# Kernel optimization log

Measured on AMD Instinct MI355X. Metric: run time of the kernel, lower is better.

The kernel has to match this reference:

```python
import jax, jax.numpy as jnp
import numpy as np

B = 64      # batch
T = 32      # frames per clip
H = 256     # hidden_dim
NMAX = 64   # max boxes per batch element


def _n_per_frame():
    rng = np.random.default_rng(0)
    return rng.integers(32, NMAX + 1, size=B)  # each n <= NMAX


def setup_inputs() -> dict:
    n = _n_per_frame()
    N = int(n.sum())  # total boxes across batch (~3072)
    key = jax.random.key(0)
    k1, k2, k3 = jax.random.split(key, 3)
    bbox = jax.random.uniform(k1, (N * T, 4), dtype=jnp.float32)
    W1 = jax.random.normal(k2, (4, 128), dtype=jnp.float32) * 0.5
    b1 = jnp.zeros((128,), jnp.float32)
    W2 = jax.random.normal(k3, (128, H), dtype=jnp.float32) * 0.0884  # ~1/sqrt(128)
    b2 = jnp.zeros((H,), jnp.float32)
    return {
        "bbox": bbox,
        "W1": W1, "b1": b1, "W2": W2, "b2": b2,
        "n_per_frame": jnp.asarray(n, jnp.int32),
        "n_max": NMAX,
    }


def reference(bbox, W1, b1, W2, b2, n_per_frame, n_max):
    N = bbox.shape[0] // T  # static total box count
    # tiny MLP: 4 -> 128 -> H
    pos = (jax.nn.relu(bbox @ W1 + b1) @ W2 + b2).reshape(N, T, H)
    # ragged scatter into padded (B*n_max, T, H) tensor
    frame_id = jnp.repeat(jnp.arange(B), n_per_frame, total_repeat_length=N)  # [N]
    starts = jnp.cumsum(n_per_frame) - n_per_frame                            # exclusive cumsum [B]
    local = jnp.arange(N) - starts[frame_id]                                  # slot within frame
    tgt = frame_id * n_max + local                                            # [N] unique targets
    pos_pad = jnp.zeros((B * n_max, T, H), pos.dtype).at[tgt].set(pos)
    # (B, n_max, T, H) -> (B, T, n_max, H) -> (B*T, n_max, H) -> (n_max, B*T, H)
    out = (pos_pad.reshape(B, n_max, T, H)
           .transpose(0, 2, 1, 3)
           .reshape(B * T, n_max, H)
           .transpose(1, 0, 2))
    return out
```

## Files before the change

### kernel.cpp

```cpp
#include <hip/hip_runtime.h>

#define B_ 64
#define T_ 32
#define H_ 256
#define NMAX_ 64
#define GRID 2048
#define BLOCK 256
#define HSROW 136

typedef __attribute__((ext_vector_type(8))) short short8;
typedef __attribute__((ext_vector_type(4))) float f32x4;

__device__ __forceinline__ short f2bf(float f) {
    unsigned u = __builtin_bit_cast(unsigned, f);
    u = (u + 0x7fffu + ((u >> 16) & 1u)) >> 16;
    return (short)u;
}

__device__ __forceinline__ void barrier_nodrain() {
    asm volatile("s_waitcnt lgkmcnt(0)\n\ts_barrier" ::: "memory");
}

__global__ __launch_bounds__(BLOCK, 4)
void pe_fused(const float* __restrict__ bbox,
              const float* __restrict__ W1,
              const float* __restrict__ b1,
              const float* __restrict__ W2,
              const float* __restrict__ b2,
              const int*   __restrict__ npf,
              float* __restrict__ out,
              int NT)
{
    __shared__ float4 W1t[128];
    __shared__ float  b1s[128];
    __shared__ int    s_n[64];
    __shared__ int    s_start[64];
    __shared__ short  Hs[64 * HSROW];

    const int tid  = threadIdx.x;
    const int wave = tid >> 6;
    const int lane = tid & 63;
    const int q    = lane >> 4;
    const int m16  = lane & 15;

    const int ch = blockIdx.x & 1;
    const int p0 = blockIdx.x >> 1;

    if (tid < 128) {
        W1t[tid] = make_float4(W1[tid], W1[128 + tid], W1[256 + tid], W1[384 + tid]);
        b1s[tid] = b1[tid];
    }
    if (wave == 0) {
        int v = npf[lane];
        s_n[lane] = v;
        int s = v;
#pragma unroll
        for (int d = 1; d < 64; d <<= 1) {
            int u = __shfl_up(s, d, 64);
            if (lane >= d) s += u;
        }
        s_start[lane] = s - v;
    }

    const int colw = ch * 128 + wave * 32;
    short8 Wf[2][4];
#pragma unroll
    for (int ct = 0; ct < 2; ++ct)
#pragma unroll
        for (int kc = 0; kc < 4; ++kc) {
            short8 f;
#pragma unroll
            for (int jj = 0; jj < 8; ++jj)
                f[jj] = f2bf(W2[(kc * 32 + q * 8 + jj) * H_ + colw + ct * 16 + m16]);
            Wf[ct][kc] = f;
        }
    float4 b2v[2];
#pragma unroll
    for (int ct = 0; ct < 2; ++ct)
        b2v[ct] = *(const float4*)(b2 + colw + ct * 16 + q * 4);

    barrier_nodrain();

#pragma unroll
    for (int it = 0; it < 2; ++it) {
        const int pair = it ? (p0 + 1024) : p0;
        const int b    = pair >> 5;
        const int l0   = (pair & 31) * 2;
        const int nb   = s_n[b];

        const int ob0 = (l0 * (B_ * T_) + b * T_) * H_;
        const int ob1 = ob0 + (B_ * T_) * H_;

        if (l0 >= nb) {
            const float4 z = make_float4(0.f, 0.f, 0.f, 0.f);
            const int col = ch * 128 + (lane & 31) * 4;
#pragma unroll
            for (int j = 0; j < 8; ++j) {
                const int r = wave * 16 + j * 2 + (lane >> 5);
                float* dst = out + (r < 32 ? ob0 + r * H_ : ob1 + (r - 32) * H_) + col;
                *(float4*)dst = z;
            }
            continue;
        }

        barrier_nodrain();

        {
            const int r4 = tid >> 2;
            const int c4 = tid & 3;
            const int g  = (s_start[b] + l0) * T_ + r4;
            float4 bv = make_float4(0.f, 0.f, 0.f, 0.f);
            if (g < NT) bv = *(const float4*)(bbox + g * 4);
            short* hrow = &Hs[r4 * HSROW + c4 * 32];
#pragma unroll
            for (int w = 0; w < 4; ++w) {
                short8 hv;
#pragma unroll
                for (int jj = 0; jj < 8; ++jj) {
                    const int h = c4 * 32 + w * 8 + jj;
                    const float4 wv = W1t[h];
                    float v = b1s[h];
                    v = fmaf(bv.x, wv.x, v);
                    v = fmaf(bv.y, wv.y, v);
                    v = fmaf(bv.z, wv.z, v);
                    v = fmaf(bv.w, wv.w, v);
                    v = fmaxf(v, 0.f);
                    hv[jj] = f2bf(v);
                }
                *(short8*)(hrow + w * 8) = hv;
            }
        }
        barrier_nodrain();

        f32x4 acc[2][4];
#pragma unroll
        for (int ct = 0; ct < 2; ++ct)
#pragma unroll
            for (int rt = 0; rt < 4; ++rt)
                acc[ct][rt] = (f32x4){b2v[ct].x, b2v[ct].y, b2v[ct].z, b2v[ct].w};

#pragma unroll
        for (int kc = 0; kc < 4; ++kc) {
            short8 hf[4];
#pragma unroll
            for (int rt = 0; rt < 4; ++rt)
                hf[rt] = *(const short8*)&Hs[(rt * 16 + m16) * HSROW + kc * 32 + q * 8];
#pragma unroll
            for (int ct = 0; ct < 2; ++ct)
#pragma unroll
                for (int rt = 0; rt < 4; ++rt)
                    acc[ct][rt] = __builtin_amdgcn_mfma_f32_16x16x32_bf16(
                        Wf[ct][kc], hf[rt], acc[ct][rt], 0, 0, 0);
        }

        const bool v1 = (l0 + 1) < nb;
#pragma unroll
        for (int ct = 0; ct < 2; ++ct) {
            const int cb = colw + ct * 16 + q * 4;
#pragma unroll
            for (int rt = 0; rt < 4; ++rt) {
                const int t = (rt & 1) * 16 + m16;
                float* dst = out + (rt < 2 ? ob0 : ob1) + t * H_ + cb;
                float4 val;
                if (rt >= 2 && !v1) {
                    val = make_float4(0.f, 0.f, 0.f, 0.f);
                } else {
                    const f32x4 a = acc[ct][rt];
                    val = make_float4(a[0], a[1], a[2], a[3]);
                }
                *(float4*)dst = val;
            }
        }
    }
}

extern "C" void kernel_launch(void* const* d_in, const int* in_sizes, int n_in,
                              void* d_out, int out_size, void* d_ws, size_t ws_size,
                              hipStream_t stream)
{
    const float* bbox = (const float*)d_in[0];
    const float* W1   = (const float*)d_in[1];
    const float* b1   = (const float*)d_in[2];
    const float* W2   = (const float*)d_in[3];
    const float* b2   = (const float*)d_in[4];
    const int*   npf  = (const int*)d_in[5];
    const int NT = in_sizes[0] / 4;

    pe_fused<<<GRID, BLOCK, 0, stream>>>(bbox, W1, b1, W2, b2, npf,
                                         (float*)d_out, NT);
}
```

Before: 165.4 us.

## Use 512-thread blocks covering all hidden columns and register-resident W1

Blocks grow from 256 to 512 threads so each block covers all 256 output columns instead of splitting them across two blocks. This halves the grid and removes the duplicated first-layer MLP work per box pair. W1 and b1 now live in registers per lane (two hidden units per lane) instead of in shared memory. The first-layer results are written to shared memory as packed bf16 pairs, and the barrier moves to after the MFMA reads. Occupancy may drop because of the larger block and the extra registers, and the store pattern changes.

```diff
diff --git a/kernel.cpp b/kernel.cpp
--- a/kernel.cpp
+++ b/kernel.cpp
@@ -4,17 +4,16 @@
 #define T_ 32
 #define H_ 256
 #define NMAX_ 64
-#define GRID 2048
-#define BLOCK 256
+#define GRID 1024
+#define BLOCK 512
 #define HSROW 136
 
 typedef __attribute__((ext_vector_type(8))) short short8;
 typedef __attribute__((ext_vector_type(4))) float f32x4;
 
-__device__ __forceinline__ short f2bf(float f) {
+__device__ __forceinline__ unsigned f2bfbits(float f) {
     unsigned u = __builtin_bit_cast(unsigned, f);
-    u = (u + 0x7fffu + ((u >> 16) & 1u)) >> 16;
-    return (short)u;
+    return (u + 0x7fffu + ((u >> 16) & 1u)) >> 16;
 }
 
 __device__ __forceinline__ void barrier_nodrain() {
@@ -31,11 +30,9 @@
               float* __restrict__ out,
               int NT)
 {
-    __shared__ float4 W1t[128];
-    __shared__ float  b1s[128];
-    __shared__ int    s_n[64];
-    __shared__ int    s_start[64];
-    __shared__ short  Hs[64 * HSROW];
+    __shared__ int   s_n[64];
+    __shared__ int   s_start[64];
+    __shared__ short Hs[64 * HSROW];
 
     const int tid  = threadIdx.x;
     const int wave = tid >> 6;
@@ -43,13 +40,6 @@
     const int q    = lane >> 4;
     const int m16  = lane & 15;
 
-    const int ch = blockIdx.x & 1;
-    const int p0 = blockIdx.x >> 1;
-
-    if (tid < 128) {
-        W1t[tid] = make_float4(W1[tid], W1[128 + tid], W1[256 + tid], W1[384 + tid]);
-        b1s[tid] = b1[tid];
-    }
     if (wave == 0) {
         int v = npf[lane];
         s_n[lane] = v;
@@ -62,72 +52,76 @@
         s_start[lane] = s - v;
     }
 
-    const int colw = ch * 128 + wave * 32;
+    const int h0 = lane * 2;
+    float w1a[4], w1b[4];
+#pragma unroll
+    for (int x = 0; x < 4; ++x) {
+        w1a[x] = W1[x * 128 + h0];
+        w1b[x] = W1[x * 128 + h0 + 1];
+    }
+    const float b1a = b1[h0], b1b = b1[h0 + 1];
+
+    const int colw = wave * 32;
     short8 Wf[2][4];
 #pragma unroll
     for (int ct = 0; ct < 2; ++ct)
 #pragma unroll
         for (int kc = 0; kc < 4; ++kc) {
+            const int k0 = kc * 32 + q * 8;
             short8 f;
 #pragma unroll
             for (int jj = 0; jj < 8; ++jj)
-                f[jj] = f2bf(W2[(kc * 32 + q * 8 + jj) * H_ + colw + ct * 16 + m16]);
+                f[jj] = (short)f2bfbits(W2[(k0 + jj) * H_ + colw + ct * 16 + m16]);
             Wf[ct][kc] = f;
         }
-    float4 b2v[2];
+    float4 bq[2];
 #pragma unroll
     for (int ct = 0; ct < 2; ++ct)
-        b2v[ct] = *(const float4*)(b2 + colw + ct * 16 + q * 4);
+        bq[ct] = *(const float4*)(b2 + colw + ct * 16 + q * 4);
 
-    barrier_nodrain();
+    __syncthreads();
 
 #pragma unroll
-    for (int it = 0; it < 2; ++it) {
-        const int pair = it ? (p0 + 1024) : p0;
-        const int b    = pair >> 5;
-        const int l0   = (pair & 31) * 2;
-        const int nb   = s_n[b];
+    for (int i = 0; i < 2; ++i) {
+        const int tt = blockIdx.x + i * GRID;
+        const int b  = tt >> 5;
+        const int l0 = (tt & 31) * 2;
+        const int nb = s_n[b];
 
         const int ob0 = (l0 * (B_ * T_) + b * T_) * H_;
         const int ob1 = ob0 + (B_ * T_) * H_;
 
         if (l0 >= nb) {
             const float4 z = make_float4(0.f, 0.f, 0.f, 0.f);
-            const int col = ch * 128 + (lane & 31) * 4;
 #pragma unroll
-            for (int j = 0; j < 8; ++j) {
-                const int r = wave * 16 + j * 2 + (lane >> 5);
-                float* dst = out + (r < 32 ? ob0 + r * H_ : ob1 + (r - 32) * H_) + col;
-                *(float4*)dst = z;
+            for (int rr = 0; rr < 8; ++rr) {
+                const int r = wave * 8 + rr;
+                float* dst = out + (r < 32 ? ob0 + r * H_ : ob1 + (r - 32) * H_);
+                *(float4*)(dst + lane * 4) = z;
             }
             continue;
         }
 
-        barrier_nodrain();
-
         {
-            const int r4 = tid >> 2;
-            const int c4 = tid & 3;
-            const int g  = (s_start[b] + l0) * T_ + r4;
-            float4 bv = make_float4(0.f, 0.f, 0.f, 0.f);
-            if (g < NT) bv = *(const float4*)(bbox + g * 4);
-            short* hrow = &Hs[r4 * HSROW + c4 * 32];
+            const int gbase = (s_start[b] + l0) * T_ + wave * 8;
+            float4 bx[8];
 #pragma unroll
-            for (int w = 0; w < 4; ++w) {
-                short8 hv;
+            for (int k = 0; k < 8; ++k) {
+                const int g = gbase + k;
+                bx[k] = make_float4(0.f, 0.f, 0.f, 0.f);
+                if (g < NT) bx[k] = *(const float4*)(bbox + g * 4);
+            }
 #pragma unroll
-                for (int jj = 0; jj < 8; ++jj) {
-                    const int h = c4 * 32 + w * 8 + jj;
-                    const float4 wv = W1t[h];
-                    float v = b1s[h];
-                    v = fmaf(bv.x, wv.x, v);
-                    v = fmaf(bv.y, wv.y, v);
-                    v = fmaf(bv.z, wv.z, v);
-                    v = fmaf(bv.w, wv.w, v);
-                    v = fmaxf(v, 0.f);
-                    hv[jj] = f2bf(v);
-                }
-                *(short8*)(hrow + w * 8) = hv;
+            for (int k = 0; k < 8; ++k) {
+                const float4 bv = bx[k];
+                float va = b1a, vb = b1b;
+                va = fmaf(bv.x, w1a[0], va); vb = fmaf(bv.x, w1b[0], vb);
+                va = fmaf(bv.y, w1a[1], va); vb = fmaf(bv.y, w1b[1], vb);
+                va = fmaf(bv.z, w1a[2], va); vb = fmaf(bv.z, w1b[2], vb);
+                va = fmaf(bv.w, w1a[3], va); vb = fmaf(bv.w, w1b[3], vb);
+                va = fmaxf(va, 0.f);         vb = fmaxf(vb, 0.f);
+                const unsigned packed = f2bfbits(va) | (f2bfbits(vb) << 16);
+                *(unsigned*)&Hs[(wave * 8 + k) * HSROW + h0] = packed;
             }
         }
         barrier_nodrain();
@@ -137,7 +131,7 @@
         for (int ct = 0; ct < 2; ++ct)
 #pragma unroll
             for (int rt = 0; rt < 4; ++rt)
-                acc[ct][rt] = (f32x4){b2v[ct].x, b2v[ct].y, b2v[ct].z, b2v[ct].w};
+                acc[ct][rt] = (f32x4){bq[ct].x, bq[ct].y, bq[ct].z, bq[ct].w};
 
 #pragma unroll
         for (int kc = 0; kc < 4; ++kc) {
@@ -152,23 +146,22 @@
                     acc[ct][rt] = __builtin_amdgcn_mfma_f32_16x16x32_bf16(
                         Wf[ct][kc], hf[rt], acc[ct][rt], 0, 0, 0);
         }
+        barrier_nodrain();
 
         const bool v1 = (l0 + 1) < nb;
 #pragma unroll
-        for (int ct = 0; ct < 2; ++ct) {
-            const int cb = colw + ct * 16 + q * 4;
-#pragma unroll
-            for (int rt = 0; rt < 4; ++rt) {
-                const int t = (rt & 1) * 16 + m16;
-                float* dst = out + (rt < 2 ? ob0 : ob1) + t * H_ + cb;
-                float4 val;
-                if (rt >= 2 && !v1) {
-                    val = make_float4(0.f, 0.f, 0.f, 0.f);
-                } else {
-                    const f32x4 a = acc[ct][rt];
-                    val = make_float4(a[0], a[1], a[2], a[3]);
-                }
-                *(float4*)dst = val;
+        for (int rt = 0; rt < 4; ++rt) {
+            const int t = (rt & 1) * 16 + m16;
+            float* dst = out + (rt < 2 ? ob0 : ob1) + t * H_ + colw + q * 4;
+            if (rt >= 2 && !v1) {
+                const float4 z = make_float4(0.f, 0.f, 0.f, 0.f);
+                *(float4*)dst = z;
+                *(float4*)(dst + 16) = z;
+            } else {
+                const f32x4 a0 = acc[0][rt];
+                const f32x4 a1 = acc[1][rt];
+                *(float4*)dst        = make_float4(a0[0], a0[1], a0[2], a0[3]);
+                *(float4*)(dst + 16) = make_float4(a1[0], a1[1], a1[2], a1[3]);
             }
         }
     }
```

Measured after the change: 165.2 us. Within noise of the previous version (-0.1%).
